# Kernel optimization log

Measured on AMD Instinct MI355X. Metric: run time of the kernel, lower is better.

Reference implementation:

```python
import jax, jax.numpy as jnp
import numpy as np
import math

B, T, TE, D, H = 1, 2048, 1024, 1024, 16
HD = D // H
INF = 1e9  # infinity_proxy from the original module
INIT_SCALE = 0.02


def sinusoid_pos_emb(timesteps, dim):
    # Transformer-XL sinusoids for relative positions [timesteps-1 .. 0].
    inv_freq = 1.0 / (10000.0 ** (np.arange(0, dim, 2) / dim))
    pos_seq = np.arange(timesteps - 1, -1, -1.0)
    inp = np.einsum('i,j->ij', pos_seq, inv_freq)
    return np.concatenate([np.sin(inp), np.cos(inp)], axis=-1).astype(np.float32)


def relative_shift(x):
    # x: [b, h, t, T] -> TXL left-pad / reshape / slice shift trick.
    b, h, t1, t2 = x.shape
    x = jnp.pad(x, ((0, 0), (0, 0), (0, 0), (1, 0)))
    x = x.reshape(b, h, t2 + 1, t1)[:, :, 1:, :]
    return x.reshape(b, h, t1, t2)


def setup_inputs() -> dict:
    key = jax.random.key(0)
    ks = jax.random.split(key, 12)
    s = INIT_SCALE
    x = jax.random.normal(ks[0], (B, T, D), jnp.float32)
    extra = jax.random.normal(ks[1], (B, TE, D), jnp.float32)
    # causal mask over the in-sequence keys; full visibility on the extra memory
    mask = jnp.broadcast_to(jnp.tril(jnp.ones((T, T), jnp.float32))[None, None], (B, 1, T, T))
    extra_mask = jnp.ones((B, 1, T, TE), jnp.float32)
    Wq = jax.random.normal(ks[2], (D, D), jnp.float32) * s
    Wk = jax.random.normal(ks[3], (D, D), jnp.float32) * s
    Wv = jax.random.normal(ks[4], (D, D), jnp.float32) * s
    Wek = jax.random.normal(ks[5], (D, D), jnp.float32) * s
    Wev = jax.random.normal(ks[6], (D, D), jnp.float32) * s
    Wr = jax.random.normal(ks[7], (D, D), jnp.float32) * s
    Wo = jax.random.normal(ks[8], (D, D), jnp.float32) * s
    r_w_bias = jax.random.normal(ks[9], (H, HD), jnp.float32) * s
    r_r_bias = jax.random.normal(ks[10], (H, HD), jnp.float32) * s
    return dict(x=x, extra=extra, mask=mask, extra_mask=extra_mask,
                Wq=Wq, Wk=Wk, Wv=Wv, Wek=Wek, Wev=Wev, Wr=Wr, Wo=Wo,
                r_w_bias=r_w_bias, r_r_bias=r_r_bias)


def reference(x, extra, mask, extra_mask, Wq, Wk, Wv, Wek, Wev, Wr, Wo, r_w_bias, r_r_bias):
    b, t, d = x.shape
    te = extra.shape[1]
    # conv1d(kernel=1, no bias) == matmul projections; cache_steps=0 so y == x
    q = (x @ Wq).reshape(b, t, H, HD)
    k = (x @ Wk).reshape(b, t, H, HD)
    v = (x @ Wv).reshape(b, t, H, HD)
    # Transformer-XL relative-position attend_fn
    pos = jnp.asarray(sinusoid_pos_emb(t, d))            # [t, D]
    r = (pos @ Wr).reshape(t, H, HD)                      # [t, H, HD]
    content = jnp.einsum('bthd,bThd->bhtT', q + r_w_bias, k)
    rel = relative_shift(jnp.einsum('bthd,Thd->bhtT', q + r_r_bias, r))
    attn = content + rel
    attn = attn * mask - INF * (1.0 - mask)
    # extra keys/values use plain dot-product attention (no rel-pos)
    ek = (extra @ Wek).reshape(b, te, H, HD)
    ev = (extra @ Wev).reshape(b, te, H, HD)
    eattn = jnp.einsum('bthd,bThd->bhtT', q, ek)
    eattn = eattn * extra_mask - INF * (1.0 - extra_mask)
    attn = jnp.concatenate([attn, eattn], axis=-1) * (1.0 / math.sqrt(HD))
    p = jax.nn.softmax(attn, axis=-1)
    vv = jnp.concatenate([v, ev], axis=1)                 # [b, t+te, H, HD]
    out = jnp.einsum('bhtT,bThd->bthd', p, vv).reshape(b, t, d)
    return out @ Wo  # final conv1d, with_final_bias=False
```

## Files before the change

kernel.cpp:

```cpp
#include <hip/hip_runtime.h>
#include <hip/hip_bf16.h>
#include <math.h>

#define T_LEN 2048
#define TE_LEN 1024
#define D_DIM 1024
#define H_NUM 16
#define HD_DIM 64
#define R_PAD 64

typedef unsigned short ushort;
typedef __attribute__((ext_vector_type(8))) short short8;
typedef __attribute__((ext_vector_type(4))) float f32x4;
typedef __attribute__((ext_vector_type(4))) ushort ushort4v;

__device__ __forceinline__ ushort f2b(float f) {
    unsigned u = __builtin_bit_cast(unsigned, f);
    u += 0x7fffu + ((u >> 16) & 1u);
    return (ushort)(u >> 16);
}
__device__ __forceinline__ float b2f(ushort s) {
    unsigned u = ((unsigned)s) << 16;
    return __builtin_bit_cast(float, u);
}

__device__ __forceinline__ void gld16(const ushort* g, ushort* l) {
    __builtin_amdgcn_global_load_lds(
        (const __attribute__((address_space(1))) unsigned int*)g,
        (__attribute__((address_space(3))) unsigned int*)l, 16, 0, 0);
}

union U8 { short8 v; ushort u[8]; };

__global__ void prep_kernel(const float* __restrict__ x, const float* __restrict__ extra,
                            ushort* __restrict__ pos, ushort* __restrict__ xb,
                            ushort* __restrict__ eb) {
    const int q = blockIdx.x * 256 + threadIdx.x;
    const int PQ = 524288;
    const int XQ = 1048576;
    if (q < PQ) {
        int idx = q * 4;
        int i = idx >> 10, j = idx & 1023;
        bool sinreg = (j < 512);
        int jj = sinreg ? j : j - 512;
        float p = (float)(2047 - i);
        ushort4v o;
#pragma unroll
        for (int u = 0; u < 4; u++) {
            float inv = exp2f((float)(jj + u) * -0.025952563241f);
            float fa = p * inv;
            ((ushort*)&o)[u] = f2b(sinreg ? sinf(fa) : cosf(fa));
        }
        *(ushort4v*)&pos[idx] = o;
    } else if (q < XQ) {
        int idx = (q - PQ) * 4;
        float4 v = *(const float4*)&x[idx];
        ushort4v o = {f2b(v.x), f2b(v.y), f2b(v.z), f2b(v.w)};
        *(ushort4v*)&xb[idx] = o;
    } else {
        int idx = (q - XQ) * 4;
        float4 v = *(const float4*)&extra[idx];
        ushort4v o = {f2b(v.x), f2b(v.y), f2b(v.z), f2b(v.w)};
        *(ushort4v*)&eb[idx] = o;
    }
}

__global__ __launch_bounds__(256) void transpose7_kernel(
    const float* __restrict__ W0, const float* __restrict__ W1,
    const float* __restrict__ W2, const float* __restrict__ W3,
    const float* __restrict__ W4, const float* __restrict__ W5,
    const float* __restrict__ W6, ushort* __restrict__ out,
    ushort* __restrict__ Rpad) {
    if (blockIdx.z == 7) {
        int gid = (blockIdx.y * 32 + blockIdx.x) * 256 + threadIdx.x;
        if (gid < (R_PAD * 1024) / 8) {
            short8 z = {0, 0, 0, 0, 0, 0, 0, 0};
            *(short8*)&Rpad[gid * 8] = z;
        }
        return;
    }
    const float* Ws[7] = {W0, W1, W2, W3, W4, W5, W6};
    const float* W = Ws[blockIdx.z];
    ushort* WT = out + (size_t)blockIdx.z * (1024 * 1024);
    __shared__ float tile[32][33];
    int c0 = blockIdx.x * 32, r0 = blockIdx.y * 32;
    int tid = threadIdx.x;
#pragma unroll
    for (int p = 0; p < 4; p++) {
        int idx = tid + p * 256;
        int r = idx >> 5, c = idx & 31;
        tile[r][c] = W[(size_t)(r0 + r) * D_DIM + c0 + c];
    }
    __syncthreads();
#pragma unroll
    for (int p = 0; p < 4; p++) {
        int idx = tid + p * 256;
        int r = idx >> 5, c = idx & 31;
        WT[(size_t)(c0 + r) * D_DIM + r0 + c] = f2b(tile[c][r]);
    }
}

__global__ __launch_bounds__(256) void gemm_mega(
    const ushort* __restrict__ xb, const ushort* __restrict__ posb,
    const ushort* __restrict__ eb, const ushort* __restrict__ WT,
    ushort* __restrict__ Qb, ushort* __restrict__ Kb, ushort* __restrict__ VTb,
    ushort* __restrict__ Rb, ushort* __restrict__ EKb, ushort* __restrict__ EVTb) {
    __shared__ ushort As[128 * 64];
    __shared__ ushort Bs[128 * 64];
    const int tid = threadIdx.x;
    const int lane = tid & 63, w = tid >> 6;
    const int l15 = lane & 15, quad = lane >> 4;
    const int wm = w & 1, wn = w >> 1;
    const size_t M1 = 1024 * 1024;

    int idx = blockIdx.x;
    const ushort *A, *BT;
    ushort* dst;
    int m0, nb0, nc0, ldt = 1024;
    bool transp = false;
    if (idx < 384) {
        m0 = (idx & 15) * 128; nb0 = (idx >> 4) * 128;
        A = xb; BT = WT;
        nc0 = nb0 & 1023;
        int seg = nb0 >> 10;
        if (seg == 0) dst = Qb;
        else if (seg == 1) dst = Kb;
        else { dst = VTb; transp = true; ldt = T_LEN; }
    } else if (idx < 512) {
        int i = idx - 384;
        m0 = (i & 15) * 128; nb0 = (i >> 4) * 128; nc0 = nb0;
        A = posb; BT = WT + 5 * M1; dst = Rb;
    } else {
        int i = idx - 512;
        m0 = (i & 7) * 128; nb0 = (i >> 3) * 128; nc0 = nb0 & 1023;
        A = eb; BT = WT + 3 * M1;
        if (nb0 < 1024) dst = EKb;
        else { dst = EVTb; transp = true; ldt = TE_LEN; }
    }

    f32x4 acc[16];
#pragma unroll
    for (int i = 0; i < 16; i++) acc[i] = (f32x4){0.f, 0.f, 0.f, 0.f};

    for (int k0 = 0; k0 < 1024; k0 += 64) {
        __syncthreads();
#pragma unroll
        for (int i = 0; i < 4; i++) {
            int ci = i * 256 + tid;
            int row = ci >> 3, cs = (ci & 7) ^ (row & 7);
            gld16(A + (size_t)(m0 + row) * 1024 + k0 + cs * 8, &As[(i * 32 + w * 8) * 64]);
            gld16(BT + (size_t)(nb0 + row) * 1024 + k0 + cs * 8, &Bs[(i * 32 + w * 8) * 64]);
        }
        __syncthreads();
#pragma unroll
        for (int kc = 0; kc < 2; kc++) {
            short8 bfr[4];
#pragma unroll
            for (int nf = 0; nf < 4; nf++) {
                const int row = wn * 64 + nf * 16 + l15;
                bfr[nf] = *(const short8*)&Bs[(row * 8 + ((kc * 4 + quad) ^ (row & 7))) * 8];
            }
#pragma unroll
            for (int mf = 0; mf < 4; mf++) {
                const int row = wm * 64 + mf * 16 + l15;
                short8 afr = *(const short8*)&As[(row * 8 + ((kc * 4 + quad) ^ (row & 7))) * 8];
#pragma unroll
                for (int nf = 0; nf < 4; nf++)
                    acc[mf * 4 + nf] = __builtin_amdgcn_mfma_f32_16x16x32_bf16(afr, bfr[nf], acc[mf * 4 + nf], 0, 0, 0);
            }
        }
    }

#pragma unroll
    for (int mf = 0; mf < 4; mf++) {
#pragma unroll
        for (int nf = 0; nf < 4; nf++) {
            f32x4 a = acc[mf * 4 + nf];
            const int mrow = m0 + wm * 64 + mf * 16 + quad * 4;
            const int nc = nc0 + wn * 64 + nf * 16 + l15;
            if (transp) {
                ushort4v v = {f2b(a[0]), f2b(a[1]), f2b(a[2]), f2b(a[3])};
                *(ushort4v*)&dst[(size_t)nc * ldt + mrow] = v;
            } else {
#pragma unroll
                for (int r = 0; r < 4; r++) dst[(size_t)(mrow + r) * 1024 + nc] = f2b(a[r]);
            }
        }
    }
}

__global__ __launch_bounds__(256) void gemm_wo(const ushort* __restrict__ A,
                                               const ushort* __restrict__ BT,
                                               float* __restrict__ out) {
    __shared__ ushort As[128 * 64];
    __shared__ ushort Bs[64 * 64];
    const int tid = threadIdx.x;
    const int lane = tid & 63, w = tid >> 6;
    const int l15 = lane & 15, quad = lane >> 4;
    const int wm = w & 1, wn = w >> 1;
    const int m0 = blockIdx.y * 128, n0 = blockIdx.x * 64;

    f32x4 acc[8];
#pragma unroll
    for (int i = 0; i < 8; i++) acc[i] = (f32x4){0.f, 0.f, 0.f, 0.f};

    for (int k0 = 0; k0 < 1024; k0 += 64) {
        __syncthreads();
#pragma unroll
        for (int i = 0; i < 4; i++) {
            int ci = i * 256 + tid;
            int row = ci >> 3, cs = (ci & 7) ^ (row & 7);
            gld16(A + (size_t)(m0 + row) * 1024 + k0 + cs * 8, &As[(i * 32 + w * 8) * 64]);
        }
#pragma unroll
        for (int i = 0; i < 2; i++) {
            int ci = i * 256 + tid;
            int row = ci >> 3, cs = (ci & 7) ^ (row & 7);
            gld16(BT + (size_t)(n0 + row) * 1024 + k0 + cs * 8, &Bs[(i * 32 + w * 8) * 64]);
        }
        __syncthreads();
#pragma unroll
        for (int kc = 0; kc < 2; kc++) {
            short8 bfr[2];
#pragma unroll
            for (int nf = 0; nf < 2; nf++) {
                const int row = wn * 32 + nf * 16 + l15;
                bfr[nf] = *(const short8*)&Bs[(row * 8 + ((kc * 4 + quad) ^ (row & 7))) * 8];
            }
#pragma unroll
            for (int mf = 0; mf < 4; mf++) {
                const int row = wm * 64 + mf * 16 + l15;
                short8 afr = *(const short8*)&As[(row * 8 + ((kc * 4 + quad) ^ (row & 7))) * 8];
#pragma unroll
                for (int nf = 0; nf < 2; nf++)
                    acc[mf * 2 + nf] = __builtin_amdgcn_mfma_f32_16x16x32_bf16(afr, bfr[nf], acc[mf * 2 + nf], 0, 0, 0);
            }
        }
    }

#pragma unroll
    for (int mf = 0; mf < 4; mf++) {
#pragma unroll
        for (int nf = 0; nf < 2; nf++) {
            f32x4 a = acc[mf * 2 + nf];
            const int mrow = m0 + wm * 64 + mf * 16 + quad * 4;
            const int nc = n0 + wn * 32 + nf * 16 + l15;
#pragma unroll
            for (int r = 0; r < 4; r++) out[(size_t)(mrow + r) * 1024 + nc] = a[r];
        }
    }
}

__global__ __launch_bounds__(256) void attn_kernel(
    const ushort* __restrict__ Qb, const ushort* __restrict__ Kb,
    const ushort* __restrict__ VT, const ushort* __restrict__ Rb,
    const ushort* __restrict__ EKb, const ushort* __restrict__ EVT,
    const float* __restrict__ rwb, const float* __restrict__ rrb,
    ushort* __restrict__ AOb) {
    __shared__ ushort Kst[2][32 * 64];
    __shared__ ushort Vst[2][64 * 32];
    __shared__ ushort Rst[128 * 64];
    __shared__ ushort Plds[4][16 * 40];

    const int tid = threadIdx.x;
    const int lane = tid & 63, w = tid >> 6;
    const int l15 = lane & 15, quad = lane >> 4;
    const int blk = blockIdx.x;
    const int xcd = blk & 7, rnd = blk >> 8, slot = (blk >> 3) & 31;
    const int h = xcd * 2 + rnd;
    const int qt = rnd ? slot : 31 - slot;
    const int t0 = qt * 64, tf = t0 + w * 16;
    const int hbase = h * HD_DIM;
    const int base0 = 1984 - t0;

    short8 qw[2], qr[2], qp[2];
#pragma unroll
    for (int kh = 0; kh < 2; kh++) {
        int dof = hbase + kh * 32 + quad * 8;
        U8 raw; raw.v = *(const short8*)&Qb[(size_t)(tf + l15) * D_DIM + dof];
        U8 a, b, c;
#pragma unroll
        for (int j = 0; j < 8; j++) {
            float f = b2f(raw.u[j]);
            a.u[j] = f2b((f + rwb[dof + j]) * 0.125f);
            b.u[j] = f2b((f + rrb[dof + j]) * 0.125f);
            c.u[j] = f2b(f * 0.125f);
        }
        qw[kh] = a.v; qr[kh] = b.v; qp[kh] = c.v;
    }

    float lr[4] = {0.f, 0.f, 0.f, 0.f};
    f32x4 O[4];
#pragma unroll
    for (int i = 0; i < 4; i++) O[i] = (f32x4){0.f, 0.f, 0.f, 0.f};

    const int nin = 2 * qt + 2, ntot = nin + 32;

    auto stageKV = [&](int tt2, int buf) {
        const bool ins = tt2 < nin;
        const int j0 = ins ? tt2 * 32 : (tt2 - nin) * 32;
        const ushort* ksrc = ins ? Kb : EKb;
        const ushort* vsrc = ins ? VT : EVT;
        const int ldv = ins ? T_LEN : TE_LEN;
        {
            int row = tid >> 3, cs = (tid & 7) ^ (row & 7);
            gld16(ksrc + (size_t)(j0 + row) * 1024 + hbase + cs * 8, &Kst[buf][w * 512]);
        }
        {
            int row = tid >> 2, cs = (tid & 3) ^ (row & 3);
            gld16(vsrc + (size_t)(hbase + row) * ldv + j0 + cs * 8, &Vst[buf][w * 512]);
        }
    };
    auto stageR = [&](int slotbase, int rowbase) {
        int k = tid >> 3;
        int s = slotbase + k;
        int cs = (tid & 7) ^ (s & 7);
        gld16(Rb + (size_t)(rowbase + k) * 1024 + hbase + cs * 8,
              &Rst[(slotbase + w * 8) * 64]);
    };

#pragma unroll
    for (int i = 0; i < 3; i++) {
        int ci = i * 256 + tid;
        int k = ci >> 3, cs = (ci & 7) ^ (k & 7);
        gld16(Rb + (size_t)(base0 + k) * 1024 + hbase + cs * 8, &Rst[(i * 32 + w * 8) * 64]);
    }
    stageKV(0, 0);

    int srcA[4]; bool lowcA[4];
#pragma unroll
    for (int r = 0; r < 4; r++) {
        const int m = quad * 4 + r;
        const int cb = 15 - m + l15;
        srcA[r] = (lane & 48) | (cb & 15);
        lowcA[r] = (cb < 16);
    }

#pragma unroll 1
    for (int tt = 0; tt < ntot; tt++) {
        const int b = tt & 1;
        __syncthreads();
        if (tt + 1 < ntot) {
            stageKV(tt + 1, 1 - b);
            if (tt + 1 < nin) stageR((96 + 32 * tt) & 127, base0 + 96 + 32 * tt);
        }

        const bool ins = tt < nin;
        const int j0 = tt * 32;

        f32x4 con[2];
#pragma unroll
        for (int i = 0; i < 2; i++) con[i] = (f32x4){0.f, 0.f, 0.f, 0.f};
#pragma unroll
        for (int kh = 0; kh < 2; kh++) {
            const short8* qa = ins ? &qw[kh] : &qp[kh];
#pragma unroll
            for (int nh = 0; nh < 2; nh++) {
                const int row = nh * 16 + l15;
                short8 kf = *(const short8*)&Kst[b][(row * 8 + ((kh * 4 + quad) ^ (row & 7))) * 8];
                con[nh] = __builtin_amdgcn_mfma_f32_16x16x32_bf16(*qa, kf, con[nh], 0, 0, 0);
            }
        }

        if (ins) {
            f32x4 rel[3];
#pragma unroll
            for (int i = 0; i < 3; i++) rel[i] = (f32x4){0.f, 0.f, 0.f, 0.f};
#pragma unroll
            for (int kh = 0; kh < 2; kh++)
#pragma unroll
                for (int cf = 0; cf < 3; cf++) {
                    const int s = (48 - 16 * w + 32 * tt + 16 * cf + l15) & 127;
                    short8 rf = *(const short8*)&Rst[(s * 8 + ((kh * 4 + quad) ^ (s & 7))) * 8];
                    rel[cf] = __builtin_amdgcn_mfma_f32_16x16x32_bf16(qr[kh], rf, rel[cf], 0, 0, 0);
                }
            const bool needmask = (j0 + 31 > tf);
#pragma unroll
            for (int r = 0; r < 4; r++) {
                const int m = quad * 4 + r;
                float b0 = __shfl(rel[0][r], srcA[r]);
                float b1 = __shfl(rel[1][r], srcA[r]);
                float b2 = __shfl(rel[2][r], srcA[r]);
                float rv0 = lowcA[r] ? b0 : b1, rv1 = lowcA[r] ? b1 : b2;
                float p0 = __expf(con[0][r] + rv0);
                float p1 = __expf(con[1][r] + rv1);
                if (needmask) {
                    const int t = tf + m;
                    if (j0 + l15 > t)      p0 = 0.f;
                    if (j0 + 16 + l15 > t) p1 = 0.f;
                }
                lr[r] += p0 + p1;
                Plds[w][m * 40 + l15]      = f2b(p0);
                Plds[w][m * 40 + 16 + l15] = f2b(p1);
            }
        } else {
#pragma unroll
            for (int r = 0; r < 4; r++) {
                const int m = quad * 4 + r;
                float p0 = __expf(con[0][r]);
                float p1 = __expf(con[1][r]);
                lr[r] += p0 + p1;
                Plds[w][m * 40 + l15]      = f2b(p0);
                Plds[w][m * 40 + 16 + l15] = f2b(p1);
            }
        }

        short8 pa = *(const short8*)&Plds[w][l15 * 40 + quad * 8];
#pragma unroll
        for (int df = 0; df < 4; df++) {
            const int row = df * 16 + l15;
            short8 vb = *(const short8*)&Vst[b][(row * 4 + (quad ^ (row & 3))) * 8];
            O[df] = __builtin_amdgcn_mfma_f32_16x16x32_bf16(pa, vb, O[df], 0, 0, 0);
        }
    }

#pragma unroll
    for (int r = 0; r < 4; r++) {
#pragma unroll
        for (int dd = 1; dd < 16; dd <<= 1) lr[r] += __shfl_xor(lr[r], dd);
        const float inv = 1.0f / lr[r];
#pragma unroll
        for (int df = 0; df < 4; df++)
            AOb[(size_t)(tf + quad * 4 + r) * D_DIM + hbase + df * 16 + l15] = f2b(O[df][r] * inv);
    }
}

extern "C" void kernel_launch(void* const* d_in, const int* in_sizes, int n_in,
                              void* d_out, int out_size, void* d_ws, size_t ws_size,
                              hipStream_t stream) {
    const float* x     = (const float*)d_in[0];
    const float* extra = (const float*)d_in[1];
    const float* Wq  = (const float*)d_in[4];
    const float* Wk  = (const float*)d_in[5];
    const float* Wv  = (const float*)d_in[6];
    const float* Wek = (const float*)d_in[7];
    const float* Wev = (const float*)d_in[8];
    const float* Wr  = (const float*)d_in[9];
    const float* Wo  = (const float*)d_in[10];
    const float* rwb = (const float*)d_in[11];
    const float* rrb = (const float*)d_in[12];
    float* out = (float*)d_out;

    ushort* ws = (ushort*)d_ws;
    const size_t M1 = 1024 * 1024;
    size_t o = 0;
    ushort* posb = ws + o; o += 2 * M1;
    ushort* xb   = ws + o; o += 2 * M1;
    ushort* eb   = ws + o; o += M1;
    ushort* WT   = ws + o; o += 7 * M1;
    ushort* Qb   = ws + o; o += 2 * M1;
    ushort* Kb   = ws + o; o += 2 * M1;
    ushort* VTb  = ws + o; o += 2 * M1;
    ushort* Rb   = ws + o; o += (size_t)(T_LEN + R_PAD) * 1024;
    ushort* EKb  = ws + o; o += M1;
    ushort* EVTb = ws + o; o += M1;
    ushort* AOb  = posb;

    prep_kernel<<<5120, 256, 0, stream>>>(x, extra, posb, xb, eb);
    transpose7_kernel<<<dim3(32, 32, 8), 256, 0, stream>>>(
        Wq, Wk, Wv, Wek, Wev, Wr, Wo, WT, Rb + (size_t)T_LEN * 1024);

    gemm_mega<<<640, 256, 0, stream>>>(xb, posb, eb, WT, Qb, Kb, VTb, Rb, EKb, EVTb);

    attn_kernel<<<512, 256, 0, stream>>>(Qb, Kb, VTb, Rb, EKb, EVTb, rwb, rrb, AOb);

    gemm_wo<<<dim3(16, 16), 256, 0, stream>>>(AOb, WT + 6 * M1, out);
}
```

Measured before the change: 276.2 us.

## Split attention key range across two wave groups per block and merge partials

The attention block grows from 256 to 512 threads. Two groups of four waves each take half of the in-sequence key tiles and half of the extra-memory tiles for the same 64 query rows, with separate K/V/R staging buffers in one shared LDS array. At the end, group 1 writes its unnormalized O and row sums to LDS and group 0 adds them in, normalizes, and stores. This halves the serial loop length per block and adds wave-level parallelism, at the cost of more LDS per block, an extra reduction step, and possibly lower occupancy.

```diff
diff --git a/kernel.cpp b/kernel.cpp
--- a/kernel.cpp
+++ b/kernel.cpp
@@ -251,27 +251,35 @@
     }
 }
 
-__global__ __launch_bounds__(256) void attn_kernel(
+__global__ __launch_bounds__(512) void attn_kernel(
     const ushort* __restrict__ Qb, const ushort* __restrict__ Kb,
     const ushort* __restrict__ VT, const ushort* __restrict__ Rb,
     const ushort* __restrict__ EKb, const ushort* __restrict__ EVT,
     const float* __restrict__ rwb, const float* __restrict__ rrb,
     ushort* __restrict__ AOb) {
-    __shared__ ushort Kst[2][32 * 64];
-    __shared__ ushort Vst[2][64 * 32];
-    __shared__ ushort Rst[128 * 64];
-    __shared__ ushort Plds[4][16 * 40];
+    __shared__ __align__(16) ushort lds[37888];
 
     const int tid = threadIdx.x;
     const int lane = tid & 63, w = tid >> 6;
+    const int g = w >> 2, wl = w & 3;
+    const int gtid = tid & 255;
     const int l15 = lane & 15, quad = lane >> 4;
     const int blk = blockIdx.x;
     const int xcd = blk & 7, rnd = blk >> 8, slot = (blk >> 3) & 31;
     const int h = xcd * 2 + rnd;
     const int qt = rnd ? slot : 31 - slot;
-    const int t0 = qt * 64, tf = t0 + w * 16;
+    const int t0 = qt * 64, tf = t0 + wl * 16;
     const int hbase = h * HD_DIM;
     const int base0 = 1984 - t0;
+    const int ninl = qt + 1;
+    const int ntotl = ninl + 16;
+    const int tt_s = g * ninl;
+    const int baseg = base0 + 32 * tt_s;
+
+    ushort* Kst = lds + g * 4096;
+    ushort* Vst = lds + 8192 + g * 4096;
+    ushort* Rst = lds + 16384 + g * 8192;
+    ushort* Pw  = lds + 32768 + w * 640;
 
     short8 qw[2], qr[2], qp[2];
 #pragma unroll
@@ -294,36 +302,37 @@
 #pragma unroll
     for (int i = 0; i < 4; i++) O[i] = (f32x4){0.f, 0.f, 0.f, 0.f};
 
-    const int nin = 2 * qt + 2, ntot = nin + 32;
-
-    auto stageKV = [&](int tt2, int buf) {
-        const bool ins = tt2 < nin;
-        const int j0 = ins ? tt2 * 32 : (tt2 - nin) * 32;
+    auto stageKV = [&](int i2, int buf) {
+        const bool ins = i2 < ninl;
+        const int j0 = ins ? (tt_s + i2) * 32 : (g * 16 + (i2 - ninl)) * 32;
         const ushort* ksrc = ins ? Kb : EKb;
         const ushort* vsrc = ins ? VT : EVT;
         const int ldv = ins ? T_LEN : TE_LEN;
         {
-            int row = tid >> 3, cs = (tid & 7) ^ (row & 7);
-            gld16(ksrc + (size_t)(j0 + row) * 1024 + hbase + cs * 8, &Kst[buf][w * 512]);
+            int row = gtid >> 3, cs = (gtid & 7) ^ (row & 7);
+            gld16(ksrc + (size_t)(j0 + row) * 1024 + hbase + cs * 8,
+                  &Kst[buf * 2048 + wl * 512]);
         }
         {
-            int row = tid >> 2, cs = (tid & 3) ^ (row & 3);
-            gld16(vsrc + (size_t)(hbase + row) * ldv + j0 + cs * 8, &Vst[buf][w * 512]);
+            int row = gtid >> 2, cs = (gtid & 3) ^ (row & 3);
+            gld16(vsrc + (size_t)(hbase + row) * ldv + j0 + cs * 8,
+                  &Vst[buf * 2048 + wl * 512]);
         }
     };
     auto stageR = [&](int slotbase, int rowbase) {
-        int k = tid >> 3;
+        int k = gtid >> 3;
         int s = slotbase + k;
-        int cs = (tid & 7) ^ (s & 7);
+        int cs = (gtid & 7) ^ (s & 7);
         gld16(Rb + (size_t)(rowbase + k) * 1024 + hbase + cs * 8,
-              &Rst[(slotbase + w * 8) * 64]);
+              &Rst[(slotbase + wl * 8) * 64]);
     };
 
 #pragma unroll
     for (int i = 0; i < 3; i++) {
-        int ci = i * 256 + tid;
+        int ci = i * 256 + gtid;
         int k = ci >> 3, cs = (ci & 7) ^ (k & 7);
-        gld16(Rb + (size_t)(base0 + k) * 1024 + hbase + cs * 8, &Rst[(i * 32 + w * 8) * 64]);
+        gld16(Rb + (size_t)(baseg + k) * 1024 + hbase + cs * 8,
+              &Rst[(i * 32 + wl * 8) * 64]);
     }
     stageKV(0, 0);
 
@@ -337,27 +346,27 @@
     }
 
 #pragma unroll 1
-    for (int tt = 0; tt < ntot; tt++) {
-        const int b = tt & 1;
+    for (int i = 0; i < ntotl; i++) {
+        const int b = i & 1;
         __syncthreads();
-        if (tt + 1 < ntot) {
-            stageKV(tt + 1, 1 - b);
-            if (tt + 1 < nin) stageR((96 + 32 * tt) & 127, base0 + 96 + 32 * tt);
-        }
-
-        const bool ins = tt < nin;
-        const int j0 = tt * 32;
+        if (i + 1 < ntotl) {
+            stageKV(i + 1, 1 - b);
+            if (i + 1 < ninl) stageR((96 + 32 * i) & 127, baseg + 96 + 32 * i);
+        }
+
+        const bool ins = i < ninl;
+        const int j0 = (tt_s + i) * 32;
 
         f32x4 con[2];
 #pragma unroll
-        for (int i = 0; i < 2; i++) con[i] = (f32x4){0.f, 0.f, 0.f, 0.f};
+        for (int c = 0; c < 2; c++) con[c] = (f32x4){0.f, 0.f, 0.f, 0.f};
 #pragma unroll
         for (int kh = 0; kh < 2; kh++) {
             const short8* qa = ins ? &qw[kh] : &qp[kh];
 #pragma unroll
             for (int nh = 0; nh < 2; nh++) {
                 const int row = nh * 16 + l15;
-                short8 kf = *(const short8*)&Kst[b][(row * 8 + ((kh * 4 + quad) ^ (row & 7))) * 8];
+                short8 kf = *(const short8*)&Kst[b * 2048 + (row * 8 + ((kh * 4 + quad) ^ (row & 7))) * 8];
                 con[nh] = __builtin_amdgcn_mfma_f32_16x16x32_bf16(*qa, kf, con[nh], 0, 0, 0);
             }
         }
@@ -365,12 +374,12 @@
         if (ins) {
             f32x4 rel[3];
 #pragma unroll
-            for (int i = 0; i < 3; i++) rel[i] = (f32x4){0.f, 0.f, 0.f, 0.f};
+            for (int c = 0; c < 3; c++) rel[c] = (f32x4){0.f, 0.f, 0.f, 0.f};
 #pragma unroll
             for (int kh = 0; kh < 2; kh++)
 #pragma unroll
                 for (int cf = 0; cf < 3; cf++) {
-                    const int s = (48 - 16 * w + 32 * tt + 16 * cf + l15) & 127;
+                    const int s = (48 - 16 * wl + 32 * i + 16 * cf + l15) & 127;
                     short8 rf = *(const short8*)&Rst[(s * 8 + ((kh * 4 + quad) ^ (s & 7))) * 8];
                     rel[cf] = __builtin_amdgcn_mfma_f32_16x16x32_bf16(qr[kh], rf, rel[cf], 0, 0, 0);
                 }
@@ -390,8 +399,8 @@
                     if (j0 + 16 + l15 > t) p1 = 0.f;
                 }
                 lr[r] += p0 + p1;
-                Plds[w][m * 40 + l15]      = f2b(p0);
-                Plds[w][m * 40 + 16 + l15] = f2b(p1);
+                Pw[m * 40 + l15]      = f2b(p0);
+                Pw[m * 40 + 16 + l15] = f2b(p1);
             }
         } else {
 #pragma unroll
@@ -400,28 +409,49 @@
                 float p0 = __expf(con[0][r]);
                 float p1 = __expf(con[1][r]);
                 lr[r] += p0 + p1;
-                Plds[w][m * 40 + l15]      = f2b(p0);
-                Plds[w][m * 40 + 16 + l15] = f2b(p1);
-            }
-        }
-
-        short8 pa = *(const short8*)&Plds[w][l15 * 40 + quad * 8];
+                Pw[m * 40 + l15]      = f2b(p0);
+                Pw[m * 40 + 16 + l15] = f2b(p1);
+            }
+        }
+
+        short8 pa = *(const short8*)&Pw[l15 * 40 + quad * 8];
 #pragma unroll
         for (int df = 0; df < 4; df++) {
             const int row = df * 16 + l15;
-            short8 vb = *(const short8*)&Vst[b][(row * 4 + (quad ^ (row & 3))) * 8];
+            short8 vb = *(const short8*)&Vst[b * 2048 + (row * 4 + (quad ^ (row & 3))) * 8];
             O[df] = __builtin_amdgcn_mfma_f32_16x16x32_bf16(pa, vb, O[df], 0, 0, 0);
         }
     }
 
 #pragma unroll
-    for (int r = 0; r < 4; r++) {
+    for (int r = 0; r < 4; r++)
 #pragma unroll
         for (int dd = 1; dd < 16; dd <<= 1) lr[r] += __shfl_xor(lr[r], dd);
-        const float inv = 1.0f / lr[r];
-#pragma unroll
-        for (int df = 0; df < 4; df++)
-            AOb[(size_t)(tf + quad * 4 + r) * D_DIM + hbase + df * 16 + l15] = f2b(O[df][r] * inv);
+
+    float* exch = (float*)(lds + 24576);
+    float* exl  = (float*)(lds + 4096);
+    __syncthreads();
+    if (g == 1) {
+#pragma unroll
+        for (int r = 0; r < 4; r++) {
+            const int row = wl * 16 + quad * 4 + r;
+            if (l15 == 0) exl[row] = lr[r];
+#pragma unroll
+            for (int df = 0; df < 4; df++)
+                exch[row * 65 + df * 16 + l15] = O[df][r];
+        }
+    }
+    __syncthreads();
+    if (g == 0) {
+#pragma unroll
+        for (int r = 0; r < 4; r++) {
+            const int row = wl * 16 + quad * 4 + r;
+            const float inv = 1.0f / (lr[r] + exl[row]);
+#pragma unroll
+            for (int df = 0; df < 4; df++)
+                AOb[(size_t)(t0 + row) * D_DIM + hbase + df * 16 + l15] =
+                    f2b((O[df][r] + exch[row * 65 + df * 16 + l15]) * inv);
+        }
     }
 }
 
@@ -462,7 +492,7 @@
 
     gemm_mega<<<640, 256, 0, stream>>>(xb, posb, eb, WT, Qb, Kb, VTb, Rb, EKb, EVTb);
 
-    attn_kernel<<<512, 256, 0, stream>>>(Qb, Kb, VTb, Rb, EKb, EVTb, rwb, rrb, AOb);
+    attn_kernel<<<512, 512, 0, stream>>>(Qb, Kb, VTb, Rb, EKb, EVTb, rwb, rrb, AOb);
 
     gemm_wo<<<dim3(16, 16), 256, 0, stream>>>(AOb, WT + 6 * M1, out);
 }
```

Result: no change. 272.1 us (-1.5%).

## Split attention KV range across two blocks and combine partial sums

Applied to the files above, without the earlier changes.

Each (head, query-tile) is now handled by two blocks, each covering half of the in-sequence and extra keys. The blocks write unnormalized fp32 outputs and row sums, and a new combine kernel adds the two halves and normalizes. This doubles the grid to raise occupancy and even out load on the causal triangle. It costs an extra kernel launch and an fp32 round trip through memory. It also carries one relative-position MFMA tile over from the previous iteration instead of recomputing it. Softmax has no max subtraction, so adding the partial sums stays valid.

```diff
diff --git a/kernel.cpp b/kernel.cpp
--- a/kernel.cpp
+++ b/kernel.cpp
@@ -256,22 +256,30 @@
     const ushort* __restrict__ VT, const ushort* __restrict__ Rb,
     const ushort* __restrict__ EKb, const ushort* __restrict__ EVT,
     const float* __restrict__ rwb, const float* __restrict__ rrb,
-    ushort* __restrict__ AOb) {
+    float* __restrict__ Of, float* __restrict__ lsum) {
     __shared__ ushort Kst[2][32 * 64];
     __shared__ ushort Vst[2][64 * 32];
     __shared__ ushort Rst[128 * 64];
     __shared__ ushort Plds[4][16 * 40];
 
     const int tid = threadIdx.x;
-    const int lane = tid & 63, w = tid >> 6;
+    const int lane = tid & 63, wl = tid >> 6;
     const int l15 = lane & 15, quad = lane >> 4;
     const int blk = blockIdx.x;
-    const int xcd = blk & 7, rnd = blk >> 8, slot = (blk >> 3) & 31;
+    const int xcd = blk & 7;
+    const int u = blk >> 3;
+    const int g = u & 1;
+    const int v = u >> 1;
+    const int rnd = v >> 5, qslot = v & 31;
     const int h = xcd * 2 + rnd;
-    const int qt = rnd ? slot : 31 - slot;
-    const int t0 = qt * 64, tf = t0 + w * 16;
+    const int qt = rnd ? qslot : 31 - qslot;
+    const int t0 = qt * 64, tf = t0 + wl * 16;
     const int hbase = h * HD_DIM;
     const int base0 = 1984 - t0;
+    const int ninl = qt + 1;
+    const int ntotl = ninl + 16;
+    const int tt_s = g * ninl;
+    const int baseg = base0 + 32 * tt_s;
 
     short8 qw[2], qr[2], qp[2];
 #pragma unroll
@@ -293,22 +301,21 @@
     f32x4 O[4];
 #pragma unroll
     for (int i = 0; i < 4; i++) O[i] = (f32x4){0.f, 0.f, 0.f, 0.f};
-
-    const int nin = 2 * qt + 2, ntot = nin + 32;
-
-    auto stageKV = [&](int tt2, int buf) {
-        const bool ins = tt2 < nin;
-        const int j0 = ins ? tt2 * 32 : (tt2 - nin) * 32;
+    f32x4 rel_carry = (f32x4){0.f, 0.f, 0.f, 0.f};
+
+    auto stageKV = [&](int i2, int buf) {
+        const bool ins = i2 < ninl;
+        const int j0 = ins ? (tt_s + i2) * 32 : (g * 16 + (i2 - ninl)) * 32;
         const ushort* ksrc = ins ? Kb : EKb;
         const ushort* vsrc = ins ? VT : EVT;
         const int ldv = ins ? T_LEN : TE_LEN;
         {
             int row = tid >> 3, cs = (tid & 7) ^ (row & 7);
-            gld16(ksrc + (size_t)(j0 + row) * 1024 + hbase + cs * 8, &Kst[buf][w * 512]);
+            gld16(ksrc + (size_t)(j0 + row) * 1024 + hbase + cs * 8, &Kst[buf][wl * 512]);
         }
         {
             int row = tid >> 2, cs = (tid & 3) ^ (row & 3);
-            gld16(vsrc + (size_t)(hbase + row) * ldv + j0 + cs * 8, &Vst[buf][w * 512]);
+            gld16(vsrc + (size_t)(hbase + row) * ldv + j0 + cs * 8, &Vst[buf][wl * 512]);
         }
     };
     auto stageR = [&](int slotbase, int rowbase) {
@@ -316,14 +323,14 @@
         int s = slotbase + k;
         int cs = (tid & 7) ^ (s & 7);
         gld16(Rb + (size_t)(rowbase + k) * 1024 + hbase + cs * 8,
-              &Rst[(slotbase + w * 8) * 64]);
+              &Rst[(slotbase + wl * 8) * 64]);
     };
 
 #pragma unroll
     for (int i = 0; i < 3; i++) {
         int ci = i * 256 + tid;
         int k = ci >> 3, cs = (ci & 7) ^ (k & 7);
-        gld16(Rb + (size_t)(base0 + k) * 1024 + hbase + cs * 8, &Rst[(i * 32 + w * 8) * 64]);
+        gld16(Rb + (size_t)(baseg + k) * 1024 + hbase + cs * 8, &Rst[(i * 32 + wl * 8) * 64]);
     }
     stageKV(0, 0);
 
@@ -337,20 +344,20 @@
     }
 
 #pragma unroll 1
-    for (int tt = 0; tt < ntot; tt++) {
-        const int b = tt & 1;
+    for (int i = 0; i < ntotl; i++) {
+        const int b = i & 1;
         __syncthreads();
-        if (tt + 1 < ntot) {
-            stageKV(tt + 1, 1 - b);
-            if (tt + 1 < nin) stageR((96 + 32 * tt) & 127, base0 + 96 + 32 * tt);
-        }
-
-        const bool ins = tt < nin;
-        const int j0 = tt * 32;
+        if (i + 1 < ntotl) {
+            stageKV(i + 1, 1 - b);
+            if (i + 1 < ninl) stageR((96 + 32 * i) & 127, baseg + 96 + 32 * i);
+        }
+
+        const bool ins = i < ninl;
+        const int j0 = (tt_s + i) * 32;
 
         f32x4 con[2];
 #pragma unroll
-        for (int i = 0; i < 2; i++) con[i] = (f32x4){0.f, 0.f, 0.f, 0.f};
+        for (int c = 0; c < 2; c++) con[c] = (f32x4){0.f, 0.f, 0.f, 0.f};
 #pragma unroll
         for (int kh = 0; kh < 2; kh++) {
             const short8* qa = ins ? &qw[kh] : &qp[kh];
@@ -363,24 +370,38 @@
         }
 
         if (ins) {
-            f32x4 rel[3];
-#pragma unroll
-            for (int i = 0; i < 3; i++) rel[i] = (f32x4){0.f, 0.f, 0.f, 0.f};
-#pragma unroll
-            for (int kh = 0; kh < 2; kh++)
-#pragma unroll
-                for (int cf = 0; cf < 3; cf++) {
-                    const int s = (48 - 16 * w + 32 * tt + 16 * cf + l15) & 127;
-                    short8 rf = *(const short8*)&Rst[(s * 8 + ((kh * 4 + quad) ^ (s & 7))) * 8];
-                    rel[cf] = __builtin_amdgcn_mfma_f32_16x16x32_bf16(qr[kh], rf, rel[cf], 0, 0, 0);
+            f32x4 relA, rel1, rel2;
+            rel1 = (f32x4){0.f, 0.f, 0.f, 0.f};
+            rel2 = (f32x4){0.f, 0.f, 0.f, 0.f};
+#pragma unroll
+            for (int kh = 0; kh < 2; kh++) {
+                const int s1 = (64 - 16 * wl + 32 * i + l15) & 127;
+                const int s2 = (80 - 16 * wl + 32 * i + l15) & 127;
+                short8 rf1 = *(const short8*)&Rst[(s1 * 8 + ((kh * 4 + quad) ^ (s1 & 7))) * 8];
+                short8 rf2 = *(const short8*)&Rst[(s2 * 8 + ((kh * 4 + quad) ^ (s2 & 7))) * 8];
+                rel1 = __builtin_amdgcn_mfma_f32_16x16x32_bf16(qr[kh], rf1, rel1, 0, 0, 0);
+                rel2 = __builtin_amdgcn_mfma_f32_16x16x32_bf16(qr[kh], rf2, rel2, 0, 0, 0);
+            }
+            if (i == 0) {
+                relA = (f32x4){0.f, 0.f, 0.f, 0.f};
+#pragma unroll
+                for (int kh = 0; kh < 2; kh++) {
+                    const int s0 = (48 - 16 * wl + l15) & 127;
+                    short8 rf0 = *(const short8*)&Rst[(s0 * 8 + ((kh * 4 + quad) ^ (s0 & 7))) * 8];
+                    relA = __builtin_amdgcn_mfma_f32_16x16x32_bf16(qr[kh], rf0, relA, 0, 0, 0);
                 }
+            } else {
+                relA = rel_carry;
+            }
+            rel_carry = rel2;
+
             const bool needmask = (j0 + 31 > tf);
 #pragma unroll
             for (int r = 0; r < 4; r++) {
                 const int m = quad * 4 + r;
-                float b0 = __shfl(rel[0][r], srcA[r]);
-                float b1 = __shfl(rel[1][r], srcA[r]);
-                float b2 = __shfl(rel[2][r], srcA[r]);
+                float b0 = __shfl(relA[r], srcA[r]);
+                float b1 = __shfl(rel1[r], srcA[r]);
+                float b2 = __shfl(rel2[r], srcA[r]);
                 float rv0 = lowcA[r] ? b0 : b1, rv1 = lowcA[r] ? b1 : b2;
                 float p0 = __expf(con[0][r] + rv0);
                 float p1 = __expf(con[1][r] + rv1);
@@ -390,8 +411,8 @@
                     if (j0 + 16 + l15 > t) p1 = 0.f;
                 }
                 lr[r] += p0 + p1;
-                Plds[w][m * 40 + l15]      = f2b(p0);
-                Plds[w][m * 40 + 16 + l15] = f2b(p1);
+                Plds[wl][m * 40 + l15]      = f2b(p0);
+                Plds[wl][m * 40 + 16 + l15] = f2b(p1);
             }
         } else {
 #pragma unroll
@@ -400,12 +421,12 @@
                 float p0 = __expf(con[0][r]);
                 float p1 = __expf(con[1][r]);
                 lr[r] += p0 + p1;
-                Plds[w][m * 40 + l15]      = f2b(p0);
-                Plds[w][m * 40 + 16 + l15] = f2b(p1);
-            }
-        }
-
-        short8 pa = *(const short8*)&Plds[w][l15 * 40 + quad * 8];
+                Plds[wl][m * 40 + l15]      = f2b(p0);
+                Plds[wl][m * 40 + 16 + l15] = f2b(p1);
+            }
+        }
+
+        short8 pa = *(const short8*)&Plds[wl][l15 * 40 + quad * 8];
 #pragma unroll
         for (int df = 0; df < 4; df++) {
             const int row = df * 16 + l15;
@@ -418,11 +439,27 @@
     for (int r = 0; r < 4; r++) {
 #pragma unroll
         for (int dd = 1; dd < 16; dd <<= 1) lr[r] += __shfl_xor(lr[r], dd);
-        const float inv = 1.0f / lr[r];
+        const int row = wl * 16 + quad * 4 + r;
+        if (l15 == 0) lsum[(size_t)(g * T_LEN + t0 + row) * H_NUM + h] = lr[r];
 #pragma unroll
         for (int df = 0; df < 4; df++)
-            AOb[(size_t)(tf + quad * 4 + r) * D_DIM + hbase + df * 16 + l15] = f2b(O[df][r] * inv);
-    }
+            Of[((size_t)g * T_LEN + t0 + row) * D_DIM + hbase + df * 16 + l15] = O[df][r];
+    }
+}
+
+__global__ __launch_bounds__(256) void combine_kernel(
+    const float* __restrict__ Of, const float* __restrict__ lsum,
+    ushort* __restrict__ AOb) {
+    const int q = blockIdx.x * 256 + threadIdx.x;
+    const int t = q >> 8;
+    const int h = (q & 255) >> 4;
+    const float inv = 1.0f / (lsum[(size_t)t * H_NUM + h] +
+                              lsum[(size_t)(T_LEN + t) * H_NUM + h]);
+    float4 a = *(const float4*)&Of[(size_t)q * 4];
+    float4 b = *(const float4*)&Of[(size_t)T_LEN * D_DIM + (size_t)q * 4];
+    ushort4v o = {f2b((a.x + b.x) * inv), f2b((a.y + b.y) * inv),
+                  f2b((a.z + b.z) * inv), f2b((a.w + b.w) * inv)};
+    *(ushort4v*)&AOb[(size_t)q * 4] = o;
 }
 
 extern "C" void kernel_launch(void* const* d_in, const int* in_sizes, int n_in,
@@ -455,6 +492,8 @@
     ushort* EKb  = ws + o; o += M1;
     ushort* EVTb = ws + o; o += M1;
     ushort* AOb  = posb;
+    float* Of    = (float*)(ws + 2 * M1);
+    float* lsum  = (float*)(ws + 10 * M1);
 
     prep_kernel<<<5120, 256, 0, stream>>>(x, extra, posb, xb, eb);
     transpose7_kernel<<<dim3(32, 32, 8), 256, 0, stream>>>(
@@ -462,7 +501,8 @@
 
     gemm_mega<<<640, 256, 0, stream>>>(xb, posb, eb, WT, Qb, Kb, VTb, Rb, EKb, EVTb);
 
-    attn_kernel<<<512, 256, 0, stream>>>(Qb, Kb, VTb, Rb, EKb, EVTb, rwb, rrb, AOb);
+    attn_kernel<<<1024, 256, 0, stream>>>(Qb, Kb, VTb, Rb, EKb, EVTb, rwb, rrb, Of, lsum);
+    combine_kernel<<<2048, 256, 0, stream>>>(Of, lsum, AOb);
 
     gemm_wo<<<dim3(16, 16), 256, 0, stream>>>(AOb, WT + 6 * M1, out);
 }
```

Result: faster. 264.0 us (-4.4%).
